# Kernel optimization log

Measured on AMD Instinct MI355X. Metric: run time of the kernel, lower is better.

## Reference

```python
import jax, jax.numpy as jnp
import numpy as np

N, E, D, H, A = 50000, 800000, 128, 256, 16


def setup_inputs() -> dict:
    key = jax.random.key(0)
    ks = jax.random.split(key, 16)
    s = 0.05
    return {
        "x": jax.random.normal(ks[0], (N, D), jnp.float32),
        "edge_index": jax.random.randint(ks[1], (2, E), 0, N, dtype=jnp.int32),
        "edge_attr": jax.random.normal(ks[2], (E, A), jnp.float32),
        # GCNConv 1 (input_dim -> hidden_dim): lin weight (no bias) + conv bias
        "W1": jax.random.normal(ks[3], (D, H), jnp.float32) * s,
        "b1": jnp.zeros((H,), jnp.float32),
        # GCNConv 2 (hidden_dim -> input_dim)
        "W2": jax.random.normal(ks[4], (H, D), jnp.float32) * s,
        "b2": jnp.zeros((D,), jnp.float32),
        # output_layer MLP: D -> H -> D
        "Wo1": jax.random.normal(ks[5], (D, H), jnp.float32) * s,
        "bo1": jnp.zeros((H,), jnp.float32),
        "Wo2": jax.random.normal(ks[6], (H, D), jnp.float32) * s,
        "bo2": jnp.zeros((D,), jnp.float32),
        # edge_predictor MLP: 2D+A -> H -> A
        "We1": jax.random.normal(ks[7], (2 * D + A, H), jnp.float32) * s,
        "be1": jnp.zeros((H,), jnp.float32),
        "We2": jax.random.normal(ks[8], (H, A), jnp.float32) * s,
        "be2": jnp.zeros((A,), jnp.float32),
    }


def reference(x, edge_index, edge_attr, W1, b1, W2, b2, Wo1, bo1, Wo2, bo2,
              We1, be1, We2, be2):
    n = x.shape[0]
    row, col = edge_index[0], edge_index[1]
    # GCNConv default: add self-loops, symmetric normalization deg^-1/2 A deg^-1/2
    loop = jnp.arange(n, dtype=row.dtype)
    row_f = jnp.concatenate([row, loop])
    col_f = jnp.concatenate([col, loop])
    deg = jax.ops.segment_sum(jnp.ones_like(col_f, dtype=x.dtype), col_f,
                              num_segments=n)
    dinv = jnp.where(deg > 0, jax.lax.rsqrt(jnp.maximum(deg, 1.0)), 0.0)
    norm = dinv[row_f] * dinv[col_f]  # [E+N]

    def gcn(h, W, b):
        h = h @ W                                # [n, out]
        msg = h[row_f] * norm[:, None]           # gather + scale
        agg = jax.ops.segment_sum(msg, col_f, num_segments=n)  # scatter-add
        return agg + b

    h = jax.nn.relu(gcn(x, W1, b1))
    h = jax.nn.relu(gcn(h, W2, b2))
    h = jax.nn.relu(h @ Wo1 + bo1) @ Wo2 + bo2   # output_layer MLP

    # edge predictor: gather endpoint features, concat with edge_attr, MLP
    edge_input = jnp.concatenate([h[row], h[col], edge_attr], axis=1)
    ea = jax.nn.relu(edge_input @ We1 + be1) @ We2 + be2
    return h, ea
```

## Files before the change

### kernel.cpp

```cpp
#include <hip/hip_runtime.h>
#include <hip/hip_bf16.h>

#define N_NODES 50000
#define N_EDGES 800000
#define DIM_D   128
#define DIM_H   256
#define DIM_A   16

typedef unsigned short u16;
typedef __attribute__((ext_vector_type(4))) float f4;
typedef __attribute__((ext_vector_type(8))) short s8;
typedef __attribute__((ext_vector_type(4))) short s4;
typedef __attribute__((ext_vector_type(2))) int i2;

__device__ __forceinline__ u16 f2bf(float f) {
    union { float f; unsigned u; } v; v.f = f;
    unsigned r = v.u + 0x7FFFu + ((v.u >> 16) & 1u);
    return (u16)(r >> 16);
}
__device__ __forceinline__ float bf2f(u16 s) {
    union { unsigned u; float f; } v; v.u = ((unsigned)s) << 16; return v.f;
}
__device__ __forceinline__ s8 zero_s8() {
    s8 v;
#pragma unroll
    for (int i = 0; i < 8; i++) v[i] = 0;
    return v;
}
__device__ __forceinline__ s4 pk_bf16x4(float a, float b, float c, float d) {
    __hip_bfloat162 h0 = __float22bfloat162_rn(make_float2(a, b));
    __hip_bfloat162 h1 = __float22bfloat162_rn(make_float2(c, d));
    s4 v;
    __builtin_memcpy(&v, &h0, 4);
    __builtin_memcpy(((char*)&v) + 4, &h1, 4);
    return v;
}
__device__ __forceinline__ u16 f2bf_hw(float f) {
    __hip_bfloat16 h = __float2bfloat16(f);
    u16 u; __builtin_memcpy(&u, &h, 2);
    return u;
}

__device__ __forceinline__ int pq_off(int mt, int q) {
    return (mt >> 2) * 64 + ((mt >> 1) & 1) * 32 + q * 8 + (mt & 1) * 4;
}

__global__ __launch_bounds__(256) void k_init(const float* __restrict__ W1, const float* __restrict__ W2,
                                              const float* __restrict__ Wo1, const float* __restrict__ Wo2,
                                              const float* __restrict__ We1, const float* __restrict__ We2,
                                              const float* __restrict__ be1,
                                              u16* __restrict__ W1t, u16* __restrict__ W2t,
                                              u16* __restrict__ Wo1t, u16* __restrict__ Wo2t,
                                              u16* __restrict__ Wabt, u16* __restrict__ Wct,
                                              u16* __restrict__ We2t, float* __restrict__ bpq,
                                              int* __restrict__ cnt) {
    int idx = blockIdx.x * 256 + threadIdx.x;
    if (idx < 32768) {
        int k = idx >> 8, n = idx & 255;
        W1t[n * 128 + k] = f2bf(W1[idx]);
    } else if (idx < 65536) {
        int r = idx - 32768, k = r >> 7, n = r & 127;
        W2t[n * 256 + k] = f2bf(W2[r]);
    } else if (idx < 98304) {
        int r = idx - 65536, k = r >> 8, n = r & 255;
        Wo1t[n * 128 + k] = f2bf(Wo1[r]);
    } else if (idx < 131072) {
        int r = idx - 98304, k = r >> 7, n = r & 127;
        Wo2t[n * 256 + k] = f2bf(Wo2[r]);
    } else if (idx < 163840) {
        int r = idx - 131072, k = r >> 8, n = r & 255;
        Wabt[n * 128 + k] = f2bf(We1[r]);
    } else if (idx < 196608) {
        int r = idx - 163840, k = r >> 8, n = r & 255;
        Wabt[32768 + n * 128 + k] = f2bf(We1[32768 + r]);
    } else if (idx < 200704) {
        int r = idx - 196608, k = r >> 8, n = r & 255;
        Wct[n * 16 + k] = f2bf(We1[65536 + r]);
    } else if (idx < 204800) {
        int r = idx - 200704, k = r >> 4, n = r & 15;
        We2t[n * 256 + k] = f2bf(We2[r]);
    } else if (idx < 205312) {
        int i = idx - 204800;
        bpq[i] = (i < 256) ? be1[i] : 0.f;
    } else if (idx < 205312 + N_NODES) {
        cnt[idx - 205312] = 0;
    }
}

__global__ __launch_bounds__(256) void k_count(const int* __restrict__ coli, int* __restrict__ cnt) {
    int e = blockIdx.x * 256 + threadIdx.x;
    if (e < N_EDGES) atomicAdd(&cnt[__builtin_nontemporal_load(&coli[e])], 1);
}

#define SCAN_C 49
__global__ __launch_bounds__(1024) void k_scan(const int* __restrict__ cnt, int* __restrict__ start,
                                               int* __restrict__ cursor) {
    __shared__ int ps[1024];
    int t = threadIdx.x;
    int base = t * SCAN_C;
    int sum = 0;
    for (int i = 0; i < SCAN_C; i++) {
        int idx = base + i;
        sum += (idx < N_NODES) ? cnt[idx] : 0;
    }
    ps[t] = sum;
    __syncthreads();
    for (int ofs = 1; ofs < 1024; ofs <<= 1) {
        int v = (t >= ofs) ? ps[t - ofs] : 0;
        __syncthreads();
        ps[t] += v;
        __syncthreads();
    }
    int run = (t > 0) ? ps[t - 1] : 0;
    for (int i = 0; i < SCAN_C; i++) {
        int idx = base + i;
        if (idx < N_NODES) {
            start[idx] = run;
            cursor[idx] = run;
            run += cnt[idx];
        }
    }
    if (t == 1023) start[N_NODES] = ps[1023];
}

__global__ __launch_bounds__(256) void k_fill(const int* __restrict__ rowi, const int* __restrict__ coli,
                                              const int* __restrict__ cnt,
                                              int* __restrict__ cursor, int2* __restrict__ pack,
                                              int2* __restrict__ eidx) {
    int e = blockIdx.x * 256 + threadIdx.x;
    if (e >= N_EDGES) return;
    int r = __builtin_nontemporal_load(&rowi[e]);
    int c = __builtin_nontemporal_load(&coli[e]);
    int slot = atomicAdd(&cursor[c], 1);
    float w = rsqrtf((float)(cnt[r] + 1)) * rsqrtf((float)(cnt[c] + 1));
    pack[slot] = make_int2(r, __float_as_int(w));
    eidx[slot] = make_int2(e, c);
}

__global__ __launch_bounds__(256) void k_cast(const float* __restrict__ X, u16* __restrict__ Y, int n4) {
    int i = blockIdx.x * 256 + threadIdx.x;
    if (i >= n4) return;
    f4 v = __builtin_nontemporal_load((const f4*)&X[(size_t)i * 4]);
    ushort4 o;
    o.x = f2bf(v[0]); o.y = f2bf(v[1]); o.z = f2bf(v[2]); o.w = f2bf(v[3]);
    *(ushort4*)&Y[(size_t)i * 4] = o;
}

template <bool OB>
__global__ __launch_bounds__(256) void k_gather(const u16* __restrict__ X,
                                                const int2* __restrict__ pack,
                                                const int* __restrict__ start,
                                                const int* __restrict__ cnt,
                                                void* __restrict__ zout) {
    int node = blockIdx.x * 4 + (threadIdx.x >> 6);
    if (node >= N_NODES) return;
    int lane = threadIdx.x & 63;
    int half = lane >> 5, j = lane & 31;
    int c4 = j * 4;
    float di = rsqrtf((float)(cnt[node] + 1));
    f4 acc = {0.f, 0.f, 0.f, 0.f};
    if (half == 0) {
        float sl = di * di;
        ushort4 u = *(const ushort4*)&X[(size_t)node * DIM_D + c4];
        acc[0] = bf2f(u.x) * sl; acc[1] = bf2f(u.y) * sl;
        acc[2] = bf2f(u.z) * sl; acc[3] = bf2f(u.w) * sl;
    }
    int s0 = start[node], e0 = start[node + 1];
    int h0 = (e0 - s0 + 1) >> 1;
    int i   = half ? (s0 + h0) : s0;
    int end = half ? e0 : (s0 + h0);
    for (; i + 3 < end; i += 4) {
        i2 p0 = __builtin_nontemporal_load((const i2*)&pack[i]);
        i2 p1 = __builtin_nontemporal_load((const i2*)&pack[i + 1]);
        i2 p2 = __builtin_nontemporal_load((const i2*)&pack[i + 2]);
        i2 p3 = __builtin_nontemporal_load((const i2*)&pack[i + 3]);
        ushort4 u0 = *(const ushort4*)&X[(size_t)p0[0] * DIM_D + c4];
        ushort4 u1 = *(const ushort4*)&X[(size_t)p1[0] * DIM_D + c4];
        ushort4 u2 = *(const ushort4*)&X[(size_t)p2[0] * DIM_D + c4];
        ushort4 u3 = *(const ushort4*)&X[(size_t)p3[0] * DIM_D + c4];
        float w0 = __int_as_float(p0[1]), w1 = __int_as_float(p1[1]);
        float w2 = __int_as_float(p2[1]), w3 = __int_as_float(p3[1]);
        acc[0] += bf2f(u0.x) * w0; acc[1] += bf2f(u0.y) * w0;
        acc[2] += bf2f(u0.z) * w0; acc[3] += bf2f(u0.w) * w0;
        acc[0] += bf2f(u1.x) * w1; acc[1] += bf2f(u1.y) * w1;
        acc[2] += bf2f(u1.z) * w1; acc[3] += bf2f(u1.w) * w1;
        acc[0] += bf2f(u2.x) * w2; acc[1] += bf2f(u2.y) * w2;
        acc[2] += bf2f(u2.z) * w2; acc[3] += bf2f(u2.w) * w2;
        acc[0] += bf2f(u3.x) * w3; acc[1] += bf2f(u3.y) * w3;
        acc[2] += bf2f(u3.z) * w3; acc[3] += bf2f(u3.w) * w3;
    }
    for (; i < end; i++) {
        i2 p = __builtin_nontemporal_load((const i2*)&pack[i]);
        float w = __int_as_float(p[1]);
        ushort4 u = *(const ushort4*)&X[(size_t)p[0] * DIM_D + c4];
        acc[0] += bf2f(u.x) * w; acc[1] += bf2f(u.y) * w;
        acc[2] += bf2f(u.z) * w; acc[3] += bf2f(u.w) * w;
    }
    float t0 = acc[0] + __shfl(acc[0], j + 32);
    float t1 = acc[1] + __shfl(acc[1], j + 32);
    float t2 = acc[2] + __shfl(acc[2], j + 32);
    float t3 = acc[3] + __shfl(acc[3], j + 32);
    if (half == 0) {
        if (OB) {
            s4 o = pk_bf16x4(t0, t1, t2, t3);
            *(s4*)&((u16*)zout)[(size_t)node * DIM_D + c4] = o;
        } else {
            *(float4*)&((float*)zout)[(size_t)node * DIM_D + c4] = make_float4(t0, t1, t2, t3);
        }
    }
}

#define BM 128
#define BK 32
#define BKP 56

template <int BNv, bool A_BF16, bool PRE_BR, bool POST_RELU, bool OUT_BF16, bool PERM_PQ>
__global__ __launch_bounds__(256) void k_gemm(const void* __restrict__ Ap,
                                              const u16* __restrict__ Wt,
                                              const float* __restrict__ preB,
                                              const float* __restrict__ postB,
                                              void* __restrict__ Cp,
                                              int M, int K, int Nn) {
    constexpr int BNT = BNv / 16;
    __shared__ __align__(16) u16 As[BM * BKP];
    __shared__ __align__(16) u16 Bs[BNv * BKP];
    const int tid = threadIdx.x;
    const int wid = tid >> 6, lane = tid & 63;
    const int q = lane >> 4, l = lane & 15;
    const int bm = blockIdx.x * BM, bn = blockIdx.y * BNv;

    f4 acc[2 * BNT];
#pragma unroll
    for (int i = 0; i < 2 * BNT; i++) { f4 zz = {0.f, 0.f, 0.f, 0.f}; acc[i] = zz; }

    for (int k0 = 0; k0 < K; k0 += BK) {
        __syncthreads();
#pragma unroll
        for (int p = 0; p < BNv / 64; p++) {
            int n = (tid >> 2) + p * 64, kc = (tid & 3) * 8;
            *(int4*)&Bs[n * BKP + kc] = *(const int4*)&Wt[(size_t)(bn + n) * K + k0 + kc];
        }
        if (A_BF16) {
            const u16* A = (const u16*)Ap;
#pragma unroll
            for (int p = 0; p < 2; p++) {
                int m = (tid >> 2) + p * 64, kc = (tid & 3) * 8;
                int gm = bm + m; if (gm >= M) gm = M - 1;
                *(int4*)&As[m * BKP + kc] = *(const int4*)&A[(size_t)gm * K + k0 + kc];
            }
        } else {
            const float* A = (const float*)Ap;
#pragma unroll
            for (int p = 0; p < 4; p++) {
                int m = (tid >> 3) + p * 32, k4 = (tid & 7) * 4;
                int gm = bm + m; if (gm >= M) gm = M - 1;
                float4 v = *(const float4*)&A[(size_t)gm * K + k0 + k4];
                if (PRE_BR) {
                    const float4 pb = *(const float4*)&preB[k0 + k4];
                    v.x = fmaxf(v.x + pb.x, 0.f);
                    v.y = fmaxf(v.y + pb.y, 0.f);
                    v.z = fmaxf(v.z + pb.z, 0.f);
                    v.w = fmaxf(v.w + pb.w, 0.f);
                }
                s4 o = pk_bf16x4(v.x, v.y, v.z, v.w);
                *(s4*)&As[m * BKP + k4] = o;
            }
        }
        __syncthreads();

        s8 af[2], bf[BNT];
#pragma unroll
        for (int mt = 0; mt < 2; mt++)
            af[mt] = *(const s8*)&As[(wid * 32 + mt * 16 + l) * BKP + q * 8];
#pragma unroll
        for (int nt = 0; nt < BNT; nt++)
            bf[nt] = *(const s8*)&Bs[(nt * 16 + l) * BKP + q * 8];
#pragma unroll
        for (int mt = 0; mt < 2; mt++)
#pragma unroll
            for (int nt = 0; nt < BNT; nt++)
                acc[mt * BNT + nt] = __builtin_amdgcn_mfma_f32_16x16x32_bf16(
                    af[mt], bf[nt], acc[mt * BNT + nt], 0, 0, 0);
    }

#pragma unroll
    for (int mt = 0; mt < 2; mt++) {
#pragma unroll
        for (int nt = 0; nt < BNT; nt++) {
            int colg = bn + nt * 16 + l;
            float pb = postB ? postB[colg] : 0.0f;
            int cols = colg;
            if (PERM_PQ) {
                int w = colg & 63, mtL = w >> 4;
                cols = (colg & ~63) | (((mtL >> 1) & 1) * 32) | (((w >> 2) & 3) * 8)
                       | ((mtL & 1) * 4) | (w & 3);
            }
#pragma unroll
            for (int r = 0; r < 4; r++) {
                int rowg = bm + wid * 32 + mt * 16 + q * 4 + r;
                if (rowg < M) {
                    float v = acc[mt * BNT + nt][r] + pb;
                    if (POST_RELU) v = fmaxf(v, 0.f);
                    if (OUT_BF16)
                        ((u16*)Cp)[(size_t)rowg * Nn + cols] = f2bf_hw(v);
                    else
                        ((float*)Cp)[(size_t)rowg * Nn + cols] = v;
                }
            }
        }
    }
}

#if __has_builtin(__builtin_amdgcn_mfma_f32_16x16x16bf16_1k)
#define KEEP4(a,b,c,d) asm volatile("" :: "v"(a), "v"(b), "v"(c), "v"(d))
__global__ __launch_bounds__(256) void k_edge(const u16* __restrict__ PQ,
                                              const float* __restrict__ attr,
                                              const int2* __restrict__ pack,
                                              const int2* __restrict__ eidx,
                                              const u16* __restrict__ Wct,
                                              const u16* __restrict__ We2t,
                                              const float* __restrict__ be2,
                                              float* __restrict__ outp) {
    __shared__ __align__(16) u16 lw[16 * 64 * 8];
    const int tid = threadIdx.x, wid = tid >> 6, lane = tid & 63;
    const int q = lane >> 4, l = lane & 15;
    for (int u = tid; u < 1024; u += 256) {
        int smt = u >> 6, sq = (u >> 4) & 3, sl = u & 15;
        *(uint2*)&lw[u * 8]     = *(const uint2*)&Wct[(smt * 16 + sl) * 16 + sq * 4];
        *(uint2*)&lw[u * 8 + 4] = *(const uint2*)&We2t[sl * DIM_H + smt * 16 + sq * 4];
    }
    __syncthreads();

    const float4 be2v = *(const float4*)&be2[q * 4];
    const int NT = N_EDGES / 16;
    const int step = gridDim.x * 4;
    const int lbase = lane * 8;

    int tile = blockIdx.x * 4 + wid;
    if (tile >= NT) return;
    i2 pk = __builtin_nontemporal_load((const i2*)&pack[tile * 16 + l]);
    i2 ec = __builtin_nontemporal_load((const i2*)&eidx[tile * 16 + l]);

    for (; tile < NT; tile += step) {
        const int re = pk[0], e = ec[0], ce = ec[1];
        const u16* prow = PQ + (size_t)re * 512 + q * 8;
        const u16* qrow = PQ + (size_t)ce * 512 + 256 + q * 8;

        f4 av = __builtin_nontemporal_load((const f4*)&attr[(size_t)e * DIM_A + q * 4]);
        s8 pw[8], qw[8];
#pragma unroll
        for (int w = 0; w < 8; w++) {
            pw[w] = *(const s8*)(prow + w * 32);
            qw[w] = *(const s8*)(qrow + w * 32);
        }
        int ntile = tile + step;
        int ns = (ntile < NT) ? ntile * 16 + l : l;
        i2 pk_n = __builtin_nontemporal_load((const i2*)&pack[ns]);
        i2 ec_n = __builtin_nontemporal_load((const i2*)&eidx[ns]);
        KEEP4(pw[0], pw[1], pw[2], pw[3]);
        KEEP4(pw[4], pw[5], pw[6], pw[7]);
        KEEP4(qw[0], qw[1], qw[2], qw[3]);
        KEEP4(qw[4], qw[5], qw[6], qw[7]);
        __builtin_amdgcn_sched_barrier(0);

        s4 af = pk_bf16x4(av[0], av[1], av[2], av[3]);

        f4 acc2 = {0.f, 0.f, 0.f, 0.f};
#pragma unroll
        for (int w = 0; w < 8; w++) {
#pragma unroll
            for (int s = 0; s < 2; s++) {
                const int mt = w * 2 + s;
                s8 wf = *(const s8*)&lw[mt * 512 + lbase];
                s4 wcf = {wf[0], wf[1], wf[2], wf[3]};
                s4 wef = {wf[4], wf[5], wf[6], wf[7]};
                f4 pqs;
                pqs[0] = bf2f((u16)pw[w][s * 4 + 0]) + bf2f((u16)qw[w][s * 4 + 0]);
                pqs[1] = bf2f((u16)pw[w][s * 4 + 1]) + bf2f((u16)qw[w][s * 4 + 1]);
                pqs[2] = bf2f((u16)pw[w][s * 4 + 2]) + bf2f((u16)qw[w][s * 4 + 2]);
                pqs[3] = bf2f((u16)pw[w][s * 4 + 3]) + bf2f((u16)qw[w][s * 4 + 3]);
                f4 acc = __builtin_amdgcn_mfma_f32_16x16x16bf16_1k(wcf, af, pqs, 0, 0, 0);
                s4 uf = pk_bf16x4(fmaxf(acc[0], 0.f), fmaxf(acc[1], 0.f),
                                  fmaxf(acc[2], 0.f), fmaxf(acc[3], 0.f));
                acc2 = __builtin_amdgcn_mfma_f32_16x16x16bf16_1k(wef, uf, acc2, 0, 0, 0);
            }
        }
        f4 ov = {acc2[0] + be2v.x, acc2[1] + be2v.y, acc2[2] + be2v.z, acc2[3] + be2v.w};
        __builtin_nontemporal_store(ov, (f4*)&outp[(size_t)e * DIM_A + q * 4]);
        pk = pk_n; ec = ec_n;
    }
}
#else
#define UPAD 268
__global__ __launch_bounds__(256) void k_edge(const u16* __restrict__ PQ,
                                              const float* __restrict__ attr,
                                              const int2* __restrict__ pack,
                                              const int2* __restrict__ eidx,
                                              const u16* __restrict__ Wct,
                                              const u16* __restrict__ We2t,
                                              const float* __restrict__ be2,
                                              float* __restrict__ outp) {
    __shared__ __align__(16) u16 ub[4][16][UPAD];
    const int tid = threadIdx.x, wid = tid >> 6, lane = tid & 63;
    const int q = lane >> 4, l = lane & 15;
    const float4 be2v = *(const float4*)&be2[q * 4];
    u16(*u)[UPAD] = ub[wid];

    s8 wcf[16];
#pragma unroll
    for (int mt = 0; mt < 16; mt++) {
        wcf[mt] = zero_s8();
        if (q < 2) wcf[mt] = *(const s8*)&Wct[(mt * 16 + l) * 16 + q * 8];
    }

    for (int tile = blockIdx.x * 4 + wid; tile < N_EDGES / 16; tile += gridDim.x * 4) {
        const int s = tile * 16 + l;
        const int2 pk = pack[s];
        const int2 ec = eidx[s];
        const int re = pk.x, e = ec.x, ce = ec.y;
        const u16* prow = PQ + (size_t)re * 512;
        const u16* qrow = PQ + (size_t)ce * 512 + 256;

        s8 af = zero_s8();
        if (q < 2) {
            const float* ap = &attr[(size_t)e * DIM_A + q * 8];
            float4 a0 = *(const float4*)ap;
            float4 a1 = *(const float4*)(ap + 4);
            af[0] = (short)f2bf(a0.x); af[1] = (short)f2bf(a0.y);
            af[2] = (short)f2bf(a0.z); af[3] = (short)f2bf(a0.w);
            af[4] = (short)f2bf(a1.x); af[5] = (short)f2bf(a1.y);
            af[6] = (short)f2bf(a1.z); af[7] = (short)f2bf(a1.w);
        }

#pragma unroll
        for (int mt = 0; mt < 16; mt++) {
            f4 cz = {0.f, 0.f, 0.f, 0.f};
            f4 acc = __builtin_amdgcn_mfma_f32_16x16x32_bf16(wcf[mt], af, cz, 0, 0, 0);
            ushort4 pu = *(const ushort4*)(prow + pq_off(mt, q));
            ushort4 qu = *(const ushort4*)(qrow + pq_off(mt, q));
            float t0 = bf2f(pu.x) + bf2f(qu.x) + acc[0];
            float t1 = bf2f(pu.y) + bf2f(qu.y) + acc[1];
            float t2 = bf2f(pu.z) + bf2f(qu.z) + acc[2];
            float t3 = bf2f(pu.w) + bf2f(qu.w) + acc[3];
            ushort4 o;
            o.x = f2bf(fmaxf(t0, 0.f)); o.y = f2bf(fmaxf(t1, 0.f));
            o.z = f2bf(fmaxf(t2, 0.f)); o.w = f2bf(fmaxf(t3, 0.f));
            *(ushort4*)&u[l][mt * 16 + q * 4] = o;
        }

        f4 acc2 = {0.f, 0.f, 0.f, 0.f};
#pragma unroll
        for (int ks = 0; ks < 8; ks++) {
            s8 uf = *(const s8*)&u[l][ks * 32 + q * 8];
            s8 wf = *(const s8*)&We2t[(size_t)l * DIM_H + ks * 32 + q * 8];
            acc2 = __builtin_amdgcn_mfma_f32_16x16x32_bf16(wf, uf, acc2, 0, 0, 0);
        }
        *(float4*)&outp[(size_t)e * DIM_A + q * 4] =
            make_float4(acc2[0] + be2v.x, acc2[1] + be2v.y,
                        acc2[2] + be2v.z, acc2[3] + be2v.w);
    }
}
#endif

extern "C" void kernel_launch(void* const* d_in, const int* in_sizes, int n_in,
                              void* d_out, int out_size, void* d_ws, size_t ws_size,
                              hipStream_t stream) {
    (void)in_sizes; (void)n_in; (void)out_size; (void)ws_size;
    const float* x    = (const float*)d_in[0];
    const int*   ei   = (const int*)d_in[1];
    const float* attr = (const float*)d_in[2];
    const float* W1   = (const float*)d_in[3];
    const float* b1   = (const float*)d_in[4];
    const float* W2   = (const float*)d_in[5];
    const float* b2   = (const float*)d_in[6];
    const float* Wo1  = (const float*)d_in[7];
    const float* bo1  = (const float*)d_in[8];
    const float* Wo2  = (const float*)d_in[9];
    const float* bo2  = (const float*)d_in[10];
    const float* We1  = (const float*)d_in[11];
    const float* be1  = (const float*)d_in[12];
    const float* We2  = (const float*)d_in[13];
    const float* be2  = (const float*)d_in[14];
    const int* rowi = ei;
    const int* coli = ei + N_EDGES;

    float* hout = (float*)d_out;
    float* eout = hout + (size_t)N_NODES * DIM_D;

    char* ws = (char*)d_ws;
    size_t off = 0;
    auto nxt = [&](size_t b) -> void* {
        void* p = ws + off; off = (off + b + 255) & ~(size_t)255; return p;
    };
    int* cnt    = (int*)nxt((size_t)N_NODES * 4);
    int* startp = (int*)nxt((size_t)(N_NODES + 1) * 4);
    int* cursor = (int*)nxt((size_t)N_NODES * 4);
    int2* pack  = (int2*)nxt((size_t)N_EDGES * 8);
    int2* eidx  = (int2*)nxt((size_t)N_EDGES * 8);
    u16* W1t   = (u16*)nxt(128 * 256 * 2);
    u16* W2t   = (u16*)nxt(128 * 256 * 2);
    u16* Wo1t  = (u16*)nxt(128 * 256 * 2);
    u16* Wo2t  = (u16*)nxt(128 * 256 * 2);
    u16* Wabt  = (u16*)nxt(512 * 128 * 2);
    u16* Wct   = (u16*)nxt(256 * 16 * 2);
    u16* We2t  = (u16*)nxt(16 * 256 * 2);
    float* bpq = (float*)nxt(512 * 4);
    u16* xb    = (u16*)nxt((size_t)N_NODES * DIM_D * 2);
    float* z   = (float*)nxt((size_t)N_NODES * DIM_D * 4);
    u16* h1    = (u16*)nxt((size_t)N_NODES * DIM_H * 2);
    u16* yb    = (u16*)nxt((size_t)N_NODES * DIM_D * 2);
    u16* PQb = (u16*)z;
    u16* zb  = (u16*)z;

    const int gE = (N_EDGES + 255) / 256;

    k_init<<<(205312 + N_NODES + 255) / 256, 256, 0, stream>>>(
        W1, W2, Wo1, Wo2, We1, We2, be1,
        W1t, W2t, Wo1t, Wo2t, Wabt, Wct, We2t, bpq, cnt);

    k_count<<<gE, 256, 0, stream>>>(coli, cnt);
    k_scan<<<1, 1024, 0, stream>>>(cnt, startp, cursor);
    k_fill<<<gE, 256, 0, stream>>>(rowi, coli, cnt, cursor, pack, eidx);

    k_cast<<<(N_NODES * DIM_D / 4 + 255) / 256, 256, 0, stream>>>(x, xb, N_NODES * DIM_D / 4);

    const int gG = (N_NODES + 3) / 4;
    k_gather<true><<<gG, 256, 0, stream>>>(xb, pack, startp, cnt, zb);
    k_gemm<128, true, false, true, true, false><<<dim3(391, 2), 256, 0, stream>>>(zb, W1t, nullptr, b1, h1, N_NODES, 128, 256);
    k_gemm<64, true, false, false, true, false><<<dim3(391, 2), 256, 0, stream>>>(h1, W2t, nullptr, nullptr, yb, N_NODES, 256, 128);
    k_gather<false><<<gG, 256, 0, stream>>>(yb, pack, startp, cnt, z);
    k_gemm<128, false, true, true, true, false><<<dim3(391, 2), 256, 0, stream>>>(z, Wo1t, b2, bo1, h1, N_NODES, 128, 256);
    k_gemm<64, true, false, false, false, false><<<dim3(391, 2), 256, 0, stream>>>(h1, Wo2t, nullptr, bo2, hout, N_NODES, 256, 128);
    k_gemm<128, false, false, false, true, true><<<dim3(391, 4), 256, 0, stream>>>(hout, Wabt, nullptr, bpq, PQb, N_NODES, 128, 512);
    k_edge<<<2048, 256, 0, stream>>>(PQb, attr, pack, eidx, Wct, We2t, be2, eout);
}
```

Before: 678.9 us.

## Replace single-block prefix scan with three-pass multi-block scan

The exclusive scan over node degrees, which ran in one 1024-thread block with each thread serially handling 49 strided elements, is split into three kernels: a per-block scan, a scan of the block sums, and an offset-add pass. The aim is to spread the scan across many workgroups and replace the uncoalesced serial loops with coalesced accesses. The cost is two extra kernel launches and a small amount of extra workspace.

```diff
diff --git a/kernel.cpp b/kernel.cpp
--- a/kernel.cpp
+++ b/kernel.cpp
@@ -92,35 +92,47 @@
     if (e < N_EDGES) atomicAdd(&cnt[__builtin_nontemporal_load(&coli[e])], 1);
 }
 
-#define SCAN_C 49
-__global__ __launch_bounds__(1024) void k_scan(const int* __restrict__ cnt, int* __restrict__ start,
+#define SCAN_BLOCKS 196
+
+__global__ __launch_bounds__(256) void k_scan1(const int* __restrict__ cnt, int* __restrict__ start,
+                                               int* __restrict__ bsum) {
+    __shared__ int ps[256];
+    int t = threadIdx.x, idx = blockIdx.x * 256 + t;
+    int v = (idx < N_NODES) ? cnt[idx] : 0;
+    ps[t] = v;
+    __syncthreads();
+    for (int ofs = 1; ofs < 256; ofs <<= 1) {
+        int u = (t >= ofs) ? ps[t - ofs] : 0;
+        __syncthreads();
+        ps[t] += u;
+        __syncthreads();
+    }
+    if (idx < N_NODES) start[idx] = ps[t] - v;
+    if (t == 255) bsum[blockIdx.x] = ps[255];
+}
+__global__ __launch_bounds__(256) void k_scan2(const int* __restrict__ bsum, int* __restrict__ boff,
+                                               int* __restrict__ start) {
+    __shared__ int ps[256];
+    int t = threadIdx.x;
+    int v = (t < SCAN_BLOCKS) ? bsum[t] : 0;
+    ps[t] = v;
+    __syncthreads();
+    for (int ofs = 1; ofs < 256; ofs <<= 1) {
+        int u = (t >= ofs) ? ps[t - ofs] : 0;
+        __syncthreads();
+        ps[t] += u;
+        __syncthreads();
+    }
+    if (t < SCAN_BLOCKS) boff[t] = ps[t] - v;
+    if (t == 255) start[N_NODES] = ps[255];
+}
+__global__ __launch_bounds__(256) void k_scan3(int* __restrict__ start, const int* __restrict__ boff,
                                                int* __restrict__ cursor) {
-    __shared__ int ps[1024];
-    int t = threadIdx.x;
-    int base = t * SCAN_C;
-    int sum = 0;
-    for (int i = 0; i < SCAN_C; i++) {
-        int idx = base + i;
-        sum += (idx < N_NODES) ? cnt[idx] : 0;
-    }
-    ps[t] = sum;
-    __syncthreads();
-    for (int ofs = 1; ofs < 1024; ofs <<= 1) {
-        int v = (t >= ofs) ? ps[t - ofs] : 0;
-        __syncthreads();
-        ps[t] += v;
-        __syncthreads();
-    }
-    int run = (t > 0) ? ps[t - 1] : 0;
-    for (int i = 0; i < SCAN_C; i++) {
-        int idx = base + i;
-        if (idx < N_NODES) {
-            start[idx] = run;
-            cursor[idx] = run;
-            run += cnt[idx];
-        }
-    }
-    if (t == 1023) start[N_NODES] = ps[1023];
+    int idx = blockIdx.x * 256 + threadIdx.x;
+    if (idx >= N_NODES) return;
+    int s = start[idx] + boff[blockIdx.x];
+    start[idx] = s;
+    cursor[idx] = s;
 }
 
 __global__ __launch_bounds__(256) void k_fill(const int* __restrict__ rowi, const int* __restrict__ coli,
@@ -495,6 +507,8 @@
     int* cnt    = (int*)nxt((size_t)N_NODES * 4);
     int* startp = (int*)nxt((size_t)(N_NODES + 1) * 4);
     int* cursor = (int*)nxt((size_t)N_NODES * 4);
+    int* bsum   = (int*)nxt((size_t)SCAN_BLOCKS * 4);
+    int* boff   = (int*)nxt((size_t)SCAN_BLOCKS * 4);
     int2* pack  = (int2*)nxt((size_t)N_EDGES * 8);
     int2* eidx  = (int2*)nxt((size_t)N_EDGES * 8);
     u16* W1t   = (u16*)nxt(128 * 256 * 2);
@@ -519,7 +533,9 @@
         W1t, W2t, Wo1t, Wo2t, Wabt, Wct, We2t, bpq, cnt);
 
     k_count<<<gE, 256, 0, stream>>>(coli, cnt);
-    k_scan<<<1, 1024, 0, stream>>>(cnt, startp, cursor);
+    k_scan1<<<SCAN_BLOCKS, 256, 0, stream>>>(cnt, startp, bsum);
+    k_scan2<<<1, 256, 0, stream>>>(bsum, boff, startp);
+    k_scan3<<<SCAN_BLOCKS, 256, 0, stream>>>(startp, boff, cursor);
     k_fill<<<gE, 256, 0, stream>>>(rowi, coli, cnt, cursor, pack, eidx);
 
     k_cast<<<(N_NODES * DIM_D / 4 + 255) / 256, 256, 0, stream>>>(x, xb, N_NODES * DIM_D / 4);
```

Result: faster. 568.4 us (-16.3%).
